# Performance work log

Hardware: AMD Instinct MI355X
Metric: run time of the kernel (lower is better)

The kernel has to match this reference:

```python
import jax, jax.numpy as jnp
import numpy as np

EPS = 1e-5
K = 20

def knn_idx(x, k):
    # x: (B, C, N); returns indices of k nearest neighbors (incl. self), (B, N, k)
    xx = jnp.sum(x * x, axis=1, keepdims=True)            # (B,1,N)
    inner = -2.0 * jnp.einsum('bcn,bcm->bnm', x, x)       # (B,N,N)
    d = -jnp.swapaxes(xx, 1, 2) - inner - xx              # -||xi - xj||^2
    return jax.lax.top_k(d, k)[1]

def graph_feature(x, k):
    # x: (B, C, N) -> (B, 2C, N, k) with [neighbor - center, center]
    B, C, N = x.shape
    idx = knn_idx(x, k)                                   # (B,N,k)
    feat = jnp.swapaxes(x, 1, 2)                          # (B,N,C)
    nb = jax.vmap(lambda f, i: f[i])(feat, idx)           # (B,N,k,C) gather
    ctr = jnp.broadcast_to(feat[:, :, None, :], nb.shape)
    out = jnp.concatenate([nb - ctr, ctr], axis=-1)       # (B,N,k,2C)
    return jnp.transpose(out, (0, 3, 1, 2))

def bn(x, g, b, m, v):
    # inference-mode batchnorm over channel axis 1
    shape = (1, -1) + (1,) * (x.ndim - 2)
    inv = g / jnp.sqrt(v + EPS)
    return x * inv.reshape(shape) + (b - m * inv).reshape(shape)

def edge_block(x, W, g, b, m, v):
    f = graph_feature(x, K)                               # (B,2C,N,k)
    h = jnp.einsum('bcnk,oc->bonk', f, W)                 # 1x1 conv, no bias
    h = jax.nn.relu(bn(h, g, b, m, v))
    return jnp.max(h, axis=-1)                            # max over k -> (B,O,N)

def _forward(x, W1, W2, W3, W4, W5,
             g1, b1, m1, v1, g2, b2, m2, v2, g3, b3, m3, v3,
             g4, b4, m4, v4, g5, b5, m5, v5, g6, b6, m6, v6,
             g7, b7, m7, v7, L1W, L2W, L2b, L3W, L3b):
    x1 = edge_block(x, W1, g1, b1, m1, v1)                # (B,64,N)
    x2 = edge_block(x1, W2, g2, b2, m2, v2)               # (B,64,N)
    x3 = edge_block(x2, W3, g3, b3, m3, v3)               # (B,128,N)
    x4 = edge_block(x3, W4, g4, b4, m4, v4)               # (B,256,N)
    cat = jnp.concatenate([x1, x2, x3, x4], axis=1)       # (B,512,N)
    h = jnp.einsum('bcn,oc->bon', cat, W5)                # conv5 1x1
    h = jax.nn.relu(bn(h, g5, b5, m5, v5))
    h = jnp.max(h, axis=-1)                               # adaptive max pool -> (B,1024)
    h = jax.nn.relu(bn(h @ L1W.T, g6, b6, m6, v6))        # dropout = identity (eval)
    h = jax.nn.relu(bn(h @ L2W.T + L2b, g7, b7, m7, v7))
    return h @ L3W.T + L3b                                # (B, num_classes)

def _bn_params(keys, c):
    k0, k1, k2, k3 = keys
    g = jax.random.uniform(k0, (c,), jnp.float32, 0.5, 1.5)
    b = 0.1 * jax.random.normal(k1, (c,), jnp.float32)
    m = 0.1 * jax.random.normal(k2, (c,), jnp.float32)
    v = jax.random.uniform(k3, (c,), jnp.float32, 0.5, 1.5)
    return g, b, m, v

def setup_inputs() -> dict:
    key = jax.random.key(0)
    ks = jax.random.split(key, 40)
    d = {}
    d['x'] = jax.random.normal(ks[0], (8, 4, 1024), jnp.float32)
    def w(k, o, i):
        return jax.random.normal(k, (o, i), jnp.float32) * np.float32(np.sqrt(2.0 / i))
    d['W1'] = w(ks[1], 64, 8)
    d['W2'] = w(ks[2], 64, 128)
    d['W3'] = w(ks[3], 128, 128)
    d['W4'] = w(ks[4], 256, 256)
    d['W5'] = w(ks[5], 1024, 512)
    for i, c in enumerate([64, 64, 128, 256, 1024, 512, 256]):
        g, b, m, v = _bn_params(jax.random.split(ks[6 + i], 4), c)
        d[f'g{i+1}'], d[f'b{i+1}'], d[f'm{i+1}'], d[f'v{i+1}'] = g, b, m, v
    d['L1W'] = w(ks[20], 512, 1024)
    d['L2W'] = w(ks[21], 256, 512)
    d['L2b'] = 0.1 * jax.random.normal(ks[22], (256,), jnp.float32)
    d['L3W'] = w(ks[23], 8, 256)
    d['L3b'] = 0.1 * jax.random.normal(ks[24], (8,), jnp.float32)
    return d

def reference(x, W1, W2, W3, W4, W5,
              g1, b1, m1, v1, g2, b2, m2, v2, g3, b3, m3, v3,
              g4, b4, m4, v4, g5, b5, m5, v5, g6, b6, m6, v6,
              g7, b7, m7, v7, L1W, L2W, L2b, L3W, L3b):
    return _forward(x, W1, W2, W3, W4, W5,
                    g1, b1, m1, v1, g2, b2, m2, v2, g3, b3, m3, v3,
                    g4, b4, m4, v4, g5, b5, m5, v5, g6, b6, m6, v6,
                    g7, b7, m7, v7, L1W, L2W, L2b, L3W, L3b)
```

## Files before the change

kernel.cpp:

```cpp
#include <hip/hip_runtime.h>
#include <cstdint>

#define BB 8
#define NN 1024
#define KK 20
#define EPSV 1e-5f

typedef __attribute__((ext_vector_type(8))) short bf16x8;
typedef __attribute__((ext_vector_type(4))) float f32x4;

__device__ __forceinline__ unsigned fenc(float f) {
  unsigned u = __float_as_uint(f);
  return (u & 0x80000000u) ? ~u : (u | 0x80000000u);
}
__device__ __forceinline__ float fdec(unsigned u) {
  u = (u & 0x80000000u) ? (u & 0x7FFFFFFFu) : ~u;
  return __uint_as_float(u);
}
__device__ __forceinline__ unsigned short f2bf(float f) {
  unsigned u = __float_as_uint(f);
  unsigned r = u + 0x7FFFu + ((u >> 16) & 1u);
  return (unsigned short)(r >> 16);
}
__device__ __forceinline__ unsigned mbcnt64(unsigned long long m) {
  unsigned r = __builtin_amdgcn_mbcnt_lo((unsigned)m, 0u);
  return __builtin_amdgcn_mbcnt_hi((unsigned)(m >> 32), r);
}

template<int C>
__global__ __launch_bounds__(256) void xx_kernel(const float* __restrict__ x, float* __restrict__ xx) {
  int p = blockIdx.x * 256 + threadIdx.x;
  if (p >= BB * NN) return;
  int b = p >> 10, n = p & (NN - 1);
  const float* xb = x + (size_t)b * C * NN + n;
  float s = 0.f;
  #pragma unroll
  for (int c = 0; c < C; ++c) { float t = xb[(size_t)c * NN]; s = fmaf(t, t, s); }
  xx[p] = s;
}

template<int C>
__global__ __launch_bounds__(256) void dist_kernel(const float* __restrict__ x, const float* __restrict__ xx,
                                                   float* __restrict__ d, int b0) {
  constexpr int CC = (C < 32) ? C : 32;
  __shared__ __align__(16) float xi[CC][64];
  __shared__ __align__(16) float xj[CC][64];
  int bl = blockIdx.z, b = b0 + bl;
  int i0 = blockIdx.y * 64, j0 = blockIdx.x * 64;
  int t = threadIdx.x;
  int tj = t & 15, ti = t >> 4;
  float acc[4][4] = {};
  const float* xb = x + (size_t)b * C * NN;
  for (int c0 = 0; c0 < C; c0 += CC) {
    __syncthreads();
    for (int p = t; p < CC * 16; p += 256) {
      int cc = p >> 4, col = (p & 15) * 4;
      *reinterpret_cast<float4*>(&xi[cc][col]) =
        *reinterpret_cast<const float4*>(&xb[(size_t)(c0 + cc) * NN + i0 + col]);
      *reinterpret_cast<float4*>(&xj[cc][col]) =
        *reinterpret_cast<const float4*>(&xb[(size_t)(c0 + cc) * NN + j0 + col]);
    }
    __syncthreads();
    #pragma unroll
    for (int cc = 0; cc < CC; ++cc) {
      float4 A  = *reinterpret_cast<const float4*>(&xi[cc][ti * 4]);
      float4 Bv = *reinterpret_cast<const float4*>(&xj[cc][tj * 4]);
      float av[4] = {A.x, A.y, A.z, A.w};
      float bv[4] = {Bv.x, Bv.y, Bv.z, Bv.w};
      #pragma unroll
      for (int a = 0; a < 4; ++a)
        #pragma unroll
        for (int q = 0; q < 4; ++q)
          acc[a][q] = fmaf(av[a], bv[q], acc[a][q]);
    }
  }
  #pragma unroll
  for (int a = 0; a < 4; ++a) {
    int i = i0 + ti * 4 + a;
    float xxi = xx[b * NN + i];
    float4 o;
    o.x = 2.f * acc[a][0] - xxi - xx[b * NN + j0 + tj * 4 + 0];
    o.y = 2.f * acc[a][1] - xxi - xx[b * NN + j0 + tj * 4 + 1];
    o.z = 2.f * acc[a][2] - xxi - xx[b * NN + j0 + tj * 4 + 2];
    o.w = 2.f * acc[a][3] - xxi - xx[b * NN + j0 + tj * 4 + 3];
    *reinterpret_cast<float4*>(&d[((size_t)bl * NN + i) * NN + j0 + tj * 4]) = o;
  }
}

__global__ __launch_bounds__(256) void topk_kernel(const float* __restrict__ d, int* __restrict__ idx, int b0) {
  int t = threadIdx.x;
  int wave = t >> 6, lane = t & 63;
  int bl = blockIdx.y, b = b0 + bl;
  int i = blockIdx.x * 4 + wave;
  const float* row = d + ((size_t)bl * NN + i) * NN;

  unsigned v[16];
  #pragma unroll
  for (int p = 0; p < 4; ++p) {
    float4 f = *reinterpret_cast<const float4*>(&row[p * 256 + lane * 4]);
    v[p * 4 + 0] = fenc(f.x);
    v[p * 4 + 1] = fenc(f.y);
    v[p * 4 + 2] = fenc(f.z);
    v[p * 4 + 3] = fenc(f.w);
  }

  unsigned long long lo = 0, hi = 0xFFFFFFFFull;
  while (lo < hi) {
    unsigned long long mid = lo + ((hi - lo + 1) >> 1);
    unsigned mt = (unsigned)mid;
    int c = 0;
    #pragma unroll
    for (int e = 0; e < 16; ++e)
      c += __popcll(__ballot(v[e] >= mt));
    if (c >= KK) lo = mid; else hi = mid - 1;
  }
  unsigned T = (unsigned)lo;

  int* op = idx + ((size_t)b * NN + i) * KK;
  int base = 0, n1 = 0;
  #pragma unroll
  for (int e = 0; e < 16; ++e) {
    unsigned long long mask = __ballot(v[e] > T);
    unsigned mb = mbcnt64(mask);
    if (v[e] > T) op[base + mb] = (e >> 2) * 256 + lane * 4 + (e & 3);
    base += __popcll(mask);
  }
  n1 = base;
  int need = KK - n1;
  int neq = 0;
  #pragma unroll
  for (int e = 0; e < 16; ++e) neq += __popcll(__ballot(v[e] == T));
  if (neq == need) {
    #pragma unroll
    for (int e = 0; e < 16; ++e) {
      unsigned long long mask = __ballot(v[e] == T);
      unsigned mb = mbcnt64(mask);
      if (v[e] == T) op[base + mb] = (e >> 2) * 256 + lane * 4 + (e & 3);
      base += __popcll(mask);
    }
  } else {
    unsigned taken = 0;
    for (int s = 0; s < need; ++s) {
      int jm = 1 << 30;
      #pragma unroll
      for (int e = 0; e < 16; ++e) {
        if (v[e] == T && !((taken >> e) & 1u)) {
          int j = (e >> 2) * 256 + lane * 4 + (e & 3);
          jm = jm < j ? jm : j;
        }
      }
      #pragma unroll
      for (int st = 1; st < 64; st <<= 1) {
        int oj = __shfl_xor(jm, st);
        jm = jm < oj ? jm : oj;
      }
      if (lane == ((jm >> 2) & 63)) {
        int e = (((jm >> 8) << 2) | (jm & 3));
        taken |= 1u << e;
        op[base + s] = jm;
      }
    }
  }
}

template<int C, int O>
__global__ __launch_bounds__(256) void pgemm_kernel(const float* __restrict__ x, const float* __restrict__ W,
                                                    float* __restrict__ Plo, float* __restrict__ Phi) {
  constexpr int CC = (C < 64) ? C : 64;
  __shared__ __align__(16) float xs[CC][64];
  __shared__ __align__(16) float wls[CC][68];
  __shared__ __align__(16) float whs[CC][68];
  int b = blockIdx.z;
  int o0 = blockIdx.y * 64, n0 = blockIdx.x * 64;
  int t = threadIdx.x;
  int tn = t & 15, to = t >> 4;
  float accl[4][4] = {}, acch[4][4] = {};
  const float* xb = x + (size_t)b * C * NN;
  for (int c0 = 0; c0 < C; c0 += CC) {
    __syncthreads();
    for (int p = t; p < CC * 64; p += 256) {
      int cc = p >> 6, col = p & 63;
      xs[cc][col] = xb[(size_t)(c0 + cc) * NN + n0 + col];
    }
    for (int p = t; p < 64 * CC; p += 256) {
      int ol = p / CC, cc = p % CC;
      wls[cc][ol] = W[(size_t)(o0 + ol) * (2 * C) + c0 + cc];
      whs[cc][ol] = W[(size_t)(o0 + ol) * (2 * C) + C + c0 + cc];
    }
    __syncthreads();
    #pragma unroll
    for (int cc = 0; cc < CC; ++cc) {
      float4 X  = *reinterpret_cast<const float4*>(&xs[cc][tn * 4]);
      float4 Wl = *reinterpret_cast<const float4*>(&wls[cc][to * 4]);
      float4 Wh = *reinterpret_cast<const float4*>(&whs[cc][to * 4]);
      float xv[4] = {X.x, X.y, X.z, X.w};
      float wl[4] = {Wl.x, Wl.y, Wl.z, Wl.w};
      float wh[4] = {Wh.x, Wh.y, Wh.z, Wh.w};
      #pragma unroll
      for (int a = 0; a < 4; ++a)
        #pragma unroll
        for (int q = 0; q < 4; ++q) {
          accl[a][q] = fmaf(wl[a], xv[q], accl[a][q]);
          acch[a][q] = fmaf(wh[a], xv[q], acch[a][q]);
        }
    }
  }
  #pragma unroll
  for (int a = 0; a < 4; ++a) {
    int o = o0 + to * 4 + a;
    size_t base = ((size_t)b * O + o) * NN + n0 + tn * 4;
    float4 vl = {accl[a][0], accl[a][1], accl[a][2], accl[a][3]};
    float4 vh = {acch[a][0], acch[a][1], acch[a][2], acch[a][3]};
    *reinterpret_cast<float4*>(&Plo[base]) = vl;
    *reinterpret_cast<float4*>(&Phi[base]) = vh;
  }
}

__global__ __launch_bounds__(256) void edgemax_kernel(const float* __restrict__ Plo, const float* __restrict__ Phi,
    const int* __restrict__ idx, const float* __restrict__ g, const float* __restrict__ bt,
    const float* __restrict__ m, const float* __restrict__ v,
    float* __restrict__ xout, int O) {
  __shared__ __align__(16) float srow[2][NN];
  __shared__ __align__(16) float sphi[2][64];
  __shared__ int   sidx[64 * KK];
  __shared__ float sinv[32], ssb[32];
  int b = blockIdx.z, n0 = blockIdx.y * 64, o0 = blockIdx.x * 32;
  int t = threadIdx.x;
  if (t < 32) {
    float inv = g[o0 + t] / sqrtf(v[o0 + t] + EPSV);
    sinv[t] = inv; ssb[t] = bt[o0 + t] - m[o0 + t] * inv;
  }
  for (int p = t; p < 64 * KK; p += 256) sidx[p] = idx[((size_t)b * NN + n0) * KK + p];
  const float* plobase = Plo + (size_t)b * O * NN;
  const float* phibase = Phi + (size_t)b * O * NN;
  float4 cur0 = *reinterpret_cast<const float4*>(&plobase[(size_t)(o0 + 0) * NN + t * 4]);
  float4 cur1 = *reinterpret_cast<const float4*>(&plobase[(size_t)(o0 + 1) * NN + t * 4]);
  float4 curphi;
  if (t < 32) curphi = *reinterpret_cast<const float4*>(&phibase[(size_t)(o0 + (t >> 4)) * NN + n0 + (t & 15) * 4]);
  __syncthreads();
  int n = t >> 2, kg = t & 3;
  int j0 = sidx[n * KK + kg * 5 + 0];
  int j1 = sidx[n * KK + kg * 5 + 1];
  int j2 = sidx[n * KK + kg * 5 + 2];
  int j3 = sidx[n * KK + kg * 5 + 3];
  int j4 = sidx[n * KK + kg * 5 + 4];
  for (int oo = 0; oo < 32; oo += 2) {
    *reinterpret_cast<float4*>(&srow[0][t * 4]) = cur0;
    *reinterpret_cast<float4*>(&srow[1][t * 4]) = cur1;
    if (t < 32) *reinterpret_cast<float4*>(&sphi[t >> 4][(t & 15) * 4]) = curphi;
    if (oo < 30) {
      cur0 = *reinterpret_cast<const float4*>(&plobase[(size_t)(o0 + oo + 2) * NN + t * 4]);
      cur1 = *reinterpret_cast<const float4*>(&plobase[(size_t)(o0 + oo + 3) * NN + t * 4]);
      if (t < 32) curphi = *reinterpret_cast<const float4*>(&phibase[(size_t)(o0 + oo + 2 + (t >> 4)) * NN + n0 + (t & 15) * 4]);
    }
    __syncthreads();
    float mx0 = srow[0][j0];
    mx0 = fmaxf(mx0, srow[0][j1]);
    mx0 = fmaxf(mx0, srow[0][j2]);
    mx0 = fmaxf(mx0, srow[0][j3]);
    mx0 = fmaxf(mx0, srow[0][j4]);
    float mx1 = srow[1][j0];
    mx1 = fmaxf(mx1, srow[1][j1]);
    mx1 = fmaxf(mx1, srow[1][j2]);
    mx1 = fmaxf(mx1, srow[1][j3]);
    mx1 = fmaxf(mx1, srow[1][j4]);
    mx0 = fmaxf(mx0, __shfl_xor(mx0, 1));
    mx0 = fmaxf(mx0, __shfl_xor(mx0, 2));
    mx1 = fmaxf(mx1, __shfl_xor(mx1, 1));
    mx1 = fmaxf(mx1, __shfl_xor(mx1, 2));
    if (kg == 0) {
      float z0 = mx0 - srow[0][n0 + n] + sphi[0][n];
      float z1 = mx1 - srow[1][n0 + n] + sphi[1][n];
      xout[((size_t)b * O + o0 + oo) * NN + n0 + n]     = fmaxf(fmaf(z0, sinv[oo],     ssb[oo]),     0.f);
      xout[((size_t)b * O + o0 + oo + 1) * NN + n0 + n] = fmaxf(fmaf(z1, sinv[oo + 1], ssb[oo + 1]), 0.f);
    }
    __syncthreads();
  }
}

__global__ __launch_bounds__(256) void tcvt_kernel(const float* __restrict__ src,
    unsigned short* __restrict__ dst, int Csrc, int c0) {
  __shared__ float tile[64][65];
  int b = blockIdx.z, cb = blockIdx.y * 64, n0 = blockIdx.x * 64;
  int t = threadIdx.x;
  const float* s = src + ((size_t)b * Csrc + cb) * NN + n0;
  #pragma unroll
  for (int rr = 0; rr < 4; ++rr) {
    int r = (t >> 4) + rr * 16;
    float4 v = *reinterpret_cast<const float4*>(&s[(size_t)r * NN + (t & 15) * 4]);
    tile[r][(t & 15) * 4 + 0] = v.x;
    tile[r][(t & 15) * 4 + 1] = v.y;
    tile[r][(t & 15) * 4 + 2] = v.z;
    tile[r][(t & 15) * 4 + 3] = v.w;
  }
  __syncthreads();
  #pragma unroll
  for (int rr = 0; rr < 2; ++rr) {
    int chunk = t + 256 * rr;
    int n = chunk >> 3, cg = (chunk & 7) * 8;
    unsigned short u[8];
    #pragma unroll
    for (int j = 0; j < 8; ++j) u[j] = f2bf(tile[cg + j][n]);
    *reinterpret_cast<uint4*>(&dst[((size_t)b * NN + n0 + n) * 512 + c0 + cb + cg]) =
      *reinterpret_cast<const uint4*>(u);
  }
}

__global__ __launch_bounds__(256) void cvtw_kernel(const float* __restrict__ W, unsigned short* __restrict__ Wb) {
  int p = (blockIdx.x * 256 + threadIdx.x) * 4;
  float4 v = *reinterpret_cast<const float4*>(&W[p]);
  unsigned short u[4] = {f2bf(v.x), f2bf(v.y), f2bf(v.z), f2bf(v.w)};
  *reinterpret_cast<uint2*>(&Wb[p]) = *reinterpret_cast<const uint2*>(u);
}

__global__ __launch_bounds__(256) void pgemm4_mfma_kernel(const unsigned short* __restrict__ Xb,
    const unsigned short* __restrict__ W4b, float* __restrict__ Plo_t, float* __restrict__ Phi_t) {
  int b = blockIdx.z;
  int n0 = blockIdx.x * 128, o0 = blockIdx.y * 64;
  int t = threadIdx.x, lane = t & 63, w = t >> 6;
  int r = lane & 15, kc = lane >> 4;
  const unsigned short* A  = Xb + ((size_t)b * NN + n0 + w * 32 + r) * 512 + 128 + kc * 8;
  const unsigned short* Bw = W4b + ((size_t)(o0 + r)) * 256 + kc * 8;
  f32x4 accl0[4] = {}, accl1[4] = {}, acch0[4] = {}, acch1[4] = {};
  #pragma unroll
  for (int ks = 0; ks < 128; ks += 32) {
    bf16x8 a0 = *reinterpret_cast<const bf16x8*>(A + ks);
    bf16x8 a1 = *reinterpret_cast<const bf16x8*>(A + 16 * 512 + ks);
    #pragma unroll
    for (int j = 0; j < 4; ++j) {
      bf16x8 bl = *reinterpret_cast<const bf16x8*>(Bw + (size_t)j * 16 * 256 + ks);
      bf16x8 bh = *reinterpret_cast<const bf16x8*>(Bw + (size_t)j * 16 * 256 + 128 + ks);
      accl0[j] = __builtin_amdgcn_mfma_f32_16x16x32_bf16(a0, bl, accl0[j], 0, 0, 0);
      accl1[j] = __builtin_amdgcn_mfma_f32_16x16x32_bf16(a1, bl, accl1[j], 0, 0, 0);
      acch0[j] = __builtin_amdgcn_mfma_f32_16x16x32_bf16(a0, bh, acch0[j], 0, 0, 0);
      acch1[j] = __builtin_amdgcn_mfma_f32_16x16x32_bf16(a1, bh, acch1[j], 0, 0, 0);
    }
  }
  #pragma unroll
  for (int j = 0; j < 4; ++j) {
    #pragma unroll
    for (int reg = 0; reg < 4; ++reg) {
      size_t n_a = (size_t)b * NN + n0 + w * 32 + kc * 4 + reg;
      size_t n_b = n_a + 16;
      int oc = o0 + j * 16 + r;
      Plo_t[n_a * 256 + oc] = accl0[j][reg];
      Plo_t[n_b * 256 + oc] = accl1[j][reg];
      Phi_t[n_a * 256 + oc] = acch0[j][reg];
      Phi_t[n_b * 256 + oc] = acch1[j][reg];
    }
  }
}

__global__ __launch_bounds__(256) void edgemax4_kernel(const float* __restrict__ Plo_t,
    const float* __restrict__ Phi_t, const int* __restrict__ idx,
    const float* __restrict__ g, const float* __restrict__ bt,
    const float* __restrict__ m, const float* __restrict__ v,
    unsigned short* __restrict__ Xb) {
  int b = blockIdx.y, t = threadIdx.x;
  int n = blockIdx.x * 4 + (t >> 6);
  int oc = (t & 63) * 4;
  const int* ip = idx + ((size_t)b * NN + n) * KK;
  const float* base = Plo_t + (size_t)b * NN * 256;
  float4 mx = {-3.4e38f, -3.4e38f, -3.4e38f, -3.4e38f};
  #pragma unroll
  for (int k = 0; k < KK; ++k) {
    float4 vv = *reinterpret_cast<const float4*>(base + (size_t)ip[k] * 256 + oc);
    mx.x = fmaxf(mx.x, vv.x);
    mx.y = fmaxf(mx.y, vv.y);
    mx.z = fmaxf(mx.z, vv.z);
    mx.w = fmaxf(mx.w, vv.w);
  }
  float4 self = *reinterpret_cast<const float4*>(base + (size_t)n * 256 + oc);
  float4 ph = *reinterpret_cast<const float4*>(Phi_t + ((size_t)b * NN + n) * 256 + oc);
  float4 gg = *reinterpret_cast<const float4*>(g + oc);
  float4 bb = *reinterpret_cast<const float4*>(bt + oc);
  float4 mm = *reinterpret_cast<const float4*>(m + oc);
  float4 vv4 = *reinterpret_cast<const float4*>(v + oc);
  float mxa[4] = {mx.x, mx.y, mx.z, mx.w};
  float sfa[4] = {self.x, self.y, self.z, self.w};
  float pha[4] = {ph.x, ph.y, ph.z, ph.w};
  float ga[4] = {gg.x, gg.y, gg.z, gg.w};
  float ba[4] = {bb.x, bb.y, bb.z, bb.w};
  float ma[4] = {mm.x, mm.y, mm.z, mm.w};
  float va[4] = {vv4.x, vv4.y, vv4.z, vv4.w};
  unsigned short u[4];
  #pragma unroll
  for (int e = 0; e < 4; ++e) {
    float inv = ga[e] / sqrtf(va[e] + EPSV);
    float z = mxa[e] - sfa[e] + pha[e];
    float y = fmaxf(fmaf(z, inv, ba[e] - ma[e] * inv), 0.f);
    u[e] = f2bf(y);
  }
  *reinterpret_cast<uint2*>(&Xb[((size_t)b * NN + n) * 512 + 256 + oc]) =
    *reinterpret_cast<const uint2*>(u);
}

__global__ __launch_bounds__(256) void conv5_mfma_kernel(const unsigned short* __restrict__ Xb,
    const unsigned short* __restrict__ W5b, unsigned* __restrict__ henc) {
  int b = blockIdx.z;
  int n0 = blockIdx.x * 128, o0 = blockIdx.y * 64;
  int t = threadIdx.x, lane = t & 63, w = t >> 6;
  int r = lane & 15, kc = lane >> 4;
  const unsigned short* A = W5b + ((size_t)(o0 + r)) * 512 + kc * 8;
  const unsigned short* B = Xb + ((size_t)b * NN + n0 + w * 32 + r) * 512 + kc * 8;
  f32x4 acc00 = {}, acc01 = {}, acc10 = {}, acc11 = {};
  f32x4 acc20 = {}, acc21 = {}, acc30 = {}, acc31 = {};
  bf16x8 a0 = *reinterpret_cast<const bf16x8*>(A + 0 * 16 * 512);
  bf16x8 a1 = *reinterpret_cast<const bf16x8*>(A + 1 * 16 * 512);
  bf16x8 a2 = *reinterpret_cast<const bf16x8*>(A + 2 * 16 * 512);
  bf16x8 a3 = *reinterpret_cast<const bf16x8*>(A + 3 * 16 * 512);
  bf16x8 b0 = *reinterpret_cast<const bf16x8*>(B);
  bf16x8 b1 = *reinterpret_cast<const bf16x8*>(B + 16 * 512);
  #pragma unroll
  for (int ks = 0; ks < 512; ks += 32) {
    bf16x8 na0, na1, na2, na3, nb0, nb1;
    if (ks + 32 < 512) {
      na0 = *reinterpret_cast<const bf16x8*>(A + 0 * 16 * 512 + ks + 32);
      na1 = *reinterpret_cast<const bf16x8*>(A + 1 * 16 * 512 + ks + 32);
      na2 = *reinterpret_cast<const bf16x8*>(A + 2 * 16 * 512 + ks + 32);
      na3 = *reinterpret_cast<const bf16x8*>(A + 3 * 16 * 512 + ks + 32);
      nb0 = *reinterpret_cast<const bf16x8*>(B + ks + 32);
      nb1 = *reinterpret_cast<const bf16x8*>(B + 16 * 512 + ks + 32);
    }
    acc00 = __builtin_amdgcn_mfma_f32_16x16x32_bf16(a0, b0, acc00, 0, 0, 0);
    acc01 = __builtin_amdgcn_mfma_f32_16x16x32_bf16(a0, b1, acc01, 0, 0, 0);
    acc10 = __builtin_amdgcn_mfma_f32_16x16x32_bf16(a1, b0, acc10, 0, 0, 0);
    acc11 = __builtin_amdgcn_mfma_f32_16x16x32_bf16(a1, b1, acc11, 0, 0, 0);
    acc20 = __builtin_amdgcn_mfma_f32_16x16x32_bf16(a2, b0, acc20, 0, 0, 0);
    acc21 = __builtin_amdgcn_mfma_f32_16x16x32_bf16(a2, b1, acc21, 0, 0, 0);
    acc30 = __builtin_amdgcn_mfma_f32_16x16x32_bf16(a3, b0, acc30, 0, 0, 0);
    acc31 = __builtin_amdgcn_mfma_f32_16x16x32_bf16(a3, b1, acc31, 0, 0, 0);
    a0 = na0; a1 = na1; a2 = na2; a3 = na3; b0 = nb0; b1 = nb1;
  }
  f32x4 m0 = {fmaxf(acc00[0], acc01[0]), fmaxf(acc00[1], acc01[1]),
              fmaxf(acc00[2], acc01[2]), fmaxf(acc00[3], acc01[3])};
  f32x4 m1 = {fmaxf(acc10[0], acc11[0]), fmaxf(acc10[1], acc11[1]),
              fmaxf(acc10[2], acc11[2]), fmaxf(acc10[3], acc11[3])};
  f32x4 m2 = {fmaxf(acc20[0], acc21[0]), fmaxf(acc20[1], acc21[1]),
              fmaxf(acc20[2], acc21[2]), fmaxf(acc20[3], acc21[3])};
  f32x4 m3 = {fmaxf(acc30[0], acc31[0]), fmaxf(acc30[1], acc31[1]),
              fmaxf(acc30[2], acc31[2]), fmaxf(acc30[3], acc31[3])};
  #pragma unroll
  for (int st = 1; st < 16; st <<= 1) {
    #pragma unroll
    for (int reg = 0; reg < 4; ++reg) {
      m0[reg] = fmaxf(m0[reg], __shfl_xor(m0[reg], st));
      m1[reg] = fmaxf(m1[reg], __shfl_xor(m1[reg], st));
      m2[reg] = fmaxf(m2[reg], __shfl_xor(m2[reg], st));
      m3[reg] = fmaxf(m3[reg], __shfl_xor(m3[reg], st));
    }
  }
  if (r == 0) {
    #pragma unroll
    for (int reg = 0; reg < 4; ++reg) {
      atomicMax(&henc[b * 1024 + o0 + 0 * 16 + kc * 4 + reg], fenc(m0[reg]));
      atomicMax(&henc[b * 1024 + o0 + 1 * 16 + kc * 4 + reg], fenc(m1[reg]));
      atomicMax(&henc[b * 1024 + o0 + 2 * 16 + kc * 4 + reg], fenc(m2[reg]));
      atomicMax(&henc[b * 1024 + o0 + 3 * 16 + kc * 4 + reg], fenc(m3[reg]));
    }
  }
}

__global__ __launch_bounds__(256) void fc1_kernel(
    const unsigned* __restrict__ henc,
    const float* __restrict__ g5, const float* __restrict__ b5, const float* __restrict__ m5, const float* __restrict__ v5,
    const float* __restrict__ L1W,
    const float* __restrict__ g6, const float* __restrict__ b6, const float* __restrict__ m6, const float* __restrict__ v6,
    float* __restrict__ y1) {
  __shared__ float sh[1024];
  int b = blockIdx.y, t = threadIdx.x;
  int o0 = blockIdx.x * 64;
  for (int o = t; o < 1024; o += 256) {
    float f = fdec(henc[b * 1024 + o]);
    float inv = g5[o] / sqrtf(v5[o] + EPSV);
    sh[o] = fmaxf(fmaf(f, inv, b5[o] - m5[o] * inv), 0.f);
  }
  __syncthreads();
  int o = o0 + (t >> 2), part = t & 3;
  float acc = 0.f;
  const float4* w4 = reinterpret_cast<const float4*>(L1W + (size_t)o * 1024 + part * 256);
  const float4* h4 = reinterpret_cast<const float4*>(sh + part * 256);
  #pragma unroll 8
  for (int c = 0; c < 64; ++c) {
    float4 a = w4[c], q = h4[c];
    acc = fmaf(a.x, q.x, fmaf(a.y, q.y, fmaf(a.z, q.z, fmaf(a.w, q.w, acc))));
  }
  acc += __shfl_xor(acc, 1);
  acc += __shfl_xor(acc, 2);
  if (part == 0) {
    float inv = g6[o] / sqrtf(v6[o] + EPSV);
    y1[b * 512 + o] = fmaxf(fmaf(acc, inv, b6[o] - m6[o] * inv), 0.f);
  }
}

__global__ __launch_bounds__(256) void fc2_kernel(
    const float* __restrict__ y1,
    const float* __restrict__ L2W, const float* __restrict__ L2b,
    const float* __restrict__ g7, const float* __restrict__ b7, const float* __restrict__ m7, const float* __restrict__ v7,
    const float* __restrict__ L3W, const float* __restrict__ L3b,
    float* __restrict__ out) {
  __shared__ float sy1[512];
  __shared__ float sy2[256];
  int b = blockIdx.x, t = threadIdx.x;
  for (int o = t; o < 512; o += 256) sy1[o] = y1[b * 512 + o];
  __syncthreads();
  {
    int o = t;
    float acc = L2b[o];
    const float4* w4 = reinterpret_cast<const float4*>(L2W + (size_t)o * 512);
    const float4* q4 = reinterpret_cast<const float4*>(sy1);
    for (int c = 0; c < 128; ++c) {
      float4 a = w4[c], q = q4[c];
      acc = fmaf(a.x, q.x, fmaf(a.y, q.y, fmaf(a.z, q.z, fmaf(a.w, q.w, acc))));
    }
    float inv = g7[o] / sqrtf(v7[o] + EPSV);
    sy2[o] = fmaxf(fmaf(acc, inv, b7[o] - m7[o] * inv), 0.f);
  }
  __syncthreads();
  if (t < 8) {
    float acc = L3b[t];
    const float4* w4 = reinterpret_cast<const float4*>(L3W + (size_t)t * 256);
    const float4* q4 = reinterpret_cast<const float4*>(sy2);
    for (int c = 0; c < 64; ++c) {
      float4 a = w4[c], q = q4[c];
      acc = fmaf(a.x, q.x, fmaf(a.y, q.y, fmaf(a.z, q.z, fmaf(a.w, q.w, acc))));
    }
    out[b * 8 + t] = acc;
  }
}

extern "C" void kernel_launch(void* const* d_in, const int* in_sizes, int n_in,
                              void* d_out, int out_size, void* d_ws, size_t ws_size,
                              hipStream_t stream) {
  (void)in_sizes; (void)n_in; (void)out_size;
  const float* x   = (const float*)d_in[0];
  const float* W1  = (const float*)d_in[1];
  const float* W2  = (const float*)d_in[2];
  const float* W3  = (const float*)d_in[3];
  const float* W4  = (const float*)d_in[4];
  const float* W5  = (const float*)d_in[5];
  const float* bnp[7][4];
  for (int i = 0; i < 7; ++i)
    for (int j = 0; j < 4; ++j)
      bnp[i][j] = (const float*)d_in[6 + i * 4 + j];
  const float* L1W = (const float*)d_in[34];
  const float* L2W = (const float*)d_in[35];
  const float* L2b = (const float*)d_in[36];
  const float* L3W = (const float*)d_in[37];
  const float* L3b = (const float*)d_in[38];
  float* out = (float*)d_out;

  char* wsb = (char*)d_ws;
  size_t off = 0;
  auto alloc = [&](size_t bytes) -> void* {
    void* p = wsb + off; off += (bytes + 255) & ~(size_t)255; return p;
  };
  int*      idx  = (int*)     alloc((size_t)BB * NN * KK * 4);
  float*    xx   = (float*)   alloc((size_t)BB * NN * 4);
  float*    x1   = (float*)   alloc((size_t)BB * 64  * NN * 4);
  float*    x2   = (float*)   alloc((size_t)BB * 64  * NN * 4);
  float*    x3   = (float*)   alloc((size_t)BB * 128 * NN * 4);
  float*    Plo  = (float*)   alloc((size_t)BB * 256 * NN * 4);
  float*    Phi  = (float*)   alloc((size_t)BB * 256 * NN * 4);
  unsigned* henc = (unsigned*)alloc((size_t)BB * 1024 * 4);
  float*    y1   = (float*)   alloc((size_t)BB * 512 * 4);
  unsigned short* Xb  = (unsigned short*)alloc((size_t)BB * NN * 512 * 2);
  unsigned short* W5b = (unsigned short*)alloc((size_t)1024 * 512 * 2);
  unsigned short* W4b = (unsigned short*)alloc((size_t)256 * 256 * 2);
  size_t left = (ws_size > off) ? (ws_size - off) : 0;
  int nb = 8;
  while (nb > 1 && (size_t)nb * NN * NN * 4 > left) nb >>= 1;
  float* dbuf = (float*)(wsb + off);

  dim3 thr(256);
  #define KNN_PHASE(CIN, XIN)                                                              \
    xx_kernel<CIN><<<dim3(32), thr, 0, stream>>>(XIN, xx);                                 \
    for (int b0 = 0; b0 < BB; b0 += nb) {                                                  \
      dist_kernel<CIN><<<dim3(16, 16, nb), thr, 0, stream>>>(XIN, xx, dbuf, b0);           \
      topk_kernel<<<dim3(NN / 4, nb), thr, 0, stream>>>(dbuf, idx, b0);                    \
    }

  cvtw_kernel<<<dim3(512), thr, 0, stream>>>(W5, W5b);
  cvtw_kernel<<<dim3(64), thr, 0, stream>>>(W4, W4b);

  KNN_PHASE(4, x)
  pgemm_kernel<4, 64><<<dim3(16, 1, BB), thr, 0, stream>>>(x, W1, Plo, Phi);
  edgemax_kernel<<<dim3(2, 16, BB), thr, 0, stream>>>(Plo, Phi, idx,
      bnp[0][0], bnp[0][1], bnp[0][2], bnp[0][3], x1, 64);
  tcvt_kernel<<<dim3(16, 1, BB), thr, 0, stream>>>(x1, Xb, 64, 0);
  KNN_PHASE(64, x1)
  pgemm_kernel<64, 64><<<dim3(16, 1, BB), thr, 0, stream>>>(x1, W2, Plo, Phi);
  edgemax_kernel<<<dim3(2, 16, BB), thr, 0, stream>>>(Plo, Phi, idx,
      bnp[1][0], bnp[1][1], bnp[1][2], bnp[1][3], x2, 64);
  tcvt_kernel<<<dim3(16, 1, BB), thr, 0, stream>>>(x2, Xb, 64, 64);
  KNN_PHASE(64, x2)
  pgemm_kernel<64, 128><<<dim3(16, 2, BB), thr, 0, stream>>>(x2, W3, Plo, Phi);
  edgemax_kernel<<<dim3(4, 16, BB), thr, 0, stream>>>(Plo, Phi, idx,
      bnp[2][0], bnp[2][1], bnp[2][2], bnp[2][3], x3, 128);
  tcvt_kernel<<<dim3(16, 2, BB), thr, 0, stream>>>(x3, Xb, 128, 128);
  KNN_PHASE(128, x3)
  pgemm4_mfma_kernel<<<dim3(8, 4, BB), thr, 0, stream>>>(Xb, W4b, Plo, Phi);
  edgemax4_kernel<<<dim3(256, BB), thr, 0, stream>>>(Plo, Phi, idx,
      bnp[3][0], bnp[3][1], bnp[3][2], bnp[3][3], Xb);
  #undef KNN_PHASE

  hipMemsetAsync(henc, 0, (size_t)BB * 1024 * 4, stream);
  conv5_mfma_kernel<<<dim3(8, 16, BB), thr, 0, stream>>>(Xb, W5b, henc);

  fc1_kernel<<<dim3(8, BB), thr, 0, stream>>>(henc,
      bnp[4][0], bnp[4][1], bnp[4][2], bnp[4][3], L1W,
      bnp[5][0], bnp[5][1], bnp[5][2], bnp[5][3], y1);
  fc2_kernel<<<dim3(BB), thr, 0, stream>>>(y1,
      L2W, L2b, bnp[6][0], bnp[6][1], bnp[6][2], bnp[6][3], L3W, L3b, out);
}
```

Baseline: 437.7 us.

## Stage conv5 weight tile in LDS and preload all activation fragments

The conv5 MFMA kernel now loads the block's 64x512 bf16 weight tile into shared memory once, stored in the MFMA fragment order, so the four waves share it instead of each fetching it from global memory. Each wave also preloads all sixteen K-step activation fragments into registers up front, replacing the one-step software prefetch. This is meant to cut redundant global weight traffic and load latency stalls. In exchange it uses 64KB of LDS and many more VGPRs, with launch bounds set to one block per SM, which lowers occupancy.

```diff
diff --git a/kernel.cpp b/kernel.cpp
--- a/kernel.cpp
+++ b/kernel.cpp
@@ -395,43 +395,49 @@
     *reinterpret_cast<const uint2*>(u);
 }
 
-__global__ __launch_bounds__(256) void conv5_mfma_kernel(const unsigned short* __restrict__ Xb,
+__global__ __launch_bounds__(256, 1) void conv5_mfma_kernel(const unsigned short* __restrict__ Xb,
     const unsigned short* __restrict__ W5b, unsigned* __restrict__ henc) {
+  __shared__ __align__(16) unsigned short lA[4096 * 8];
   int b = blockIdx.z;
   int n0 = blockIdx.x * 128, o0 = blockIdx.y * 64;
   int t = threadIdx.x, lane = t & 63, w = t >> 6;
   int r = lane & 15, kc = lane >> 4;
-  const unsigned short* A = W5b + ((size_t)(o0 + r)) * 512 + kc * 8;
+
   const unsigned short* B = Xb + ((size_t)b * NN + n0 + w * 32 + r) * 512 + kc * 8;
+  bf16x8 b0[16], b1[16];
+  #pragma unroll
+  for (int ks = 0; ks < 16; ++ks) {
+    b0[ks] = *reinterpret_cast<const bf16x8*>(B + ks * 32);
+    b1[ks] = *reinterpret_cast<const bf16x8*>(B + 16 * 512 + ks * 32);
+  }
+
+  #pragma unroll
+  for (int i = 0; i < 16; ++i) {
+    int e = i * 256 + t;
+    int le = e & 63, je = (e >> 6) & 3, kse = e >> 8;
+    const unsigned short* src = W5b + ((size_t)(o0 + je * 16 + (le & 15))) * 512 + ((le >> 4) & 3) * 8 + kse * 32;
+    *reinterpret_cast<uint4*>(&lA[(size_t)e * 8]) = *reinterpret_cast<const uint4*>(src);
+  }
+  __syncthreads();
+
   f32x4 acc00 = {}, acc01 = {}, acc10 = {}, acc11 = {};
   f32x4 acc20 = {}, acc21 = {}, acc30 = {}, acc31 = {};
-  bf16x8 a0 = *reinterpret_cast<const bf16x8*>(A + 0 * 16 * 512);
-  bf16x8 a1 = *reinterpret_cast<const bf16x8*>(A + 1 * 16 * 512);
-  bf16x8 a2 = *reinterpret_cast<const bf16x8*>(A + 2 * 16 * 512);
-  bf16x8 a3 = *reinterpret_cast<const bf16x8*>(A + 3 * 16 * 512);
-  bf16x8 b0 = *reinterpret_cast<const bf16x8*>(B);
-  bf16x8 b1 = *reinterpret_cast<const bf16x8*>(B + 16 * 512);
-  #pragma unroll
-  for (int ks = 0; ks < 512; ks += 32) {
-    bf16x8 na0, na1, na2, na3, nb0, nb1;
-    if (ks + 32 < 512) {
-      na0 = *reinterpret_cast<const bf16x8*>(A + 0 * 16 * 512 + ks + 32);
-      na1 = *reinterpret_cast<const bf16x8*>(A + 1 * 16 * 512 + ks + 32);
-      na2 = *reinterpret_cast<const bf16x8*>(A + 2 * 16 * 512 + ks + 32);
-      na3 = *reinterpret_cast<const bf16x8*>(A + 3 * 16 * 512 + ks + 32);
-      nb0 = *reinterpret_cast<const bf16x8*>(B + ks + 32);
-      nb1 = *reinterpret_cast<const bf16x8*>(B + 16 * 512 + ks + 32);
-    }
-    acc00 = __builtin_amdgcn_mfma_f32_16x16x32_bf16(a0, b0, acc00, 0, 0, 0);
-    acc01 = __builtin_amdgcn_mfma_f32_16x16x32_bf16(a0, b1, acc01, 0, 0, 0);
-    acc10 = __builtin_amdgcn_mfma_f32_16x16x32_bf16(a1, b0, acc10, 0, 0, 0);
-    acc11 = __builtin_amdgcn_mfma_f32_16x16x32_bf16(a1, b1, acc11, 0, 0, 0);
-    acc20 = __builtin_amdgcn_mfma_f32_16x16x32_bf16(a2, b0, acc20, 0, 0, 0);
-    acc21 = __builtin_amdgcn_mfma_f32_16x16x32_bf16(a2, b1, acc21, 0, 0, 0);
-    acc30 = __builtin_amdgcn_mfma_f32_16x16x32_bf16(a3, b0, acc30, 0, 0, 0);
-    acc31 = __builtin_amdgcn_mfma_f32_16x16x32_bf16(a3, b1, acc31, 0, 0, 0);
-    a0 = na0; a1 = na1; a2 = na2; a3 = na3; b0 = nb0; b1 = nb1;
-  }
+  #pragma unroll
+  for (int ks = 0; ks < 16; ++ks) {
+    bf16x8 a0 = *reinterpret_cast<const bf16x8*>(&lA[(size_t)((ks * 4 + 0) * 64 + lane) * 8]);
+    bf16x8 a1 = *reinterpret_cast<const bf16x8*>(&lA[(size_t)((ks * 4 + 1) * 64 + lane) * 8]);
+    bf16x8 a2 = *reinterpret_cast<const bf16x8*>(&lA[(size_t)((ks * 4 + 2) * 64 + lane) * 8]);
+    bf16x8 a3 = *reinterpret_cast<const bf16x8*>(&lA[(size_t)((ks * 4 + 3) * 64 + lane) * 8]);
+    acc00 = __builtin_amdgcn_mfma_f32_16x16x32_bf16(a0, b0[ks], acc00, 0, 0, 0);
+    acc01 = __builtin_amdgcn_mfma_f32_16x16x32_bf16(a0, b1[ks], acc01, 0, 0, 0);
+    acc10 = __builtin_amdgcn_mfma_f32_16x16x32_bf16(a1, b0[ks], acc10, 0, 0, 0);
+    acc11 = __builtin_amdgcn_mfma_f32_16x16x32_bf16(a1, b1[ks], acc11, 0, 0, 0);
+    acc20 = __builtin_amdgcn_mfma_f32_16x16x32_bf16(a2, b0[ks], acc20, 0, 0, 0);
+    acc21 = __builtin_amdgcn_mfma_f32_16x16x32_bf16(a2, b1[ks], acc21, 0, 0, 0);
+    acc30 = __builtin_amdgcn_mfma_f32_16x16x32_bf16(a3, b0[ks], acc30, 0, 0, 0);
+    acc31 = __builtin_amdgcn_mfma_f32_16x16x32_bf16(a3, b1[ks], acc31, 0, 0, 0);
+  }
+
   f32x4 m0 = {fmaxf(acc00[0], acc01[0]), fmaxf(acc00[1], acc01[1]),
               fmaxf(acc00[2], acc01[2]), fmaxf(acc00[3], acc01[3])};
   f32x4 m1 = {fmaxf(acc10[0], acc11[0]), fmaxf(acc10[1], acc11[1]),
```

Measured after the change: 419.5 us, median of 2. 4.1% less time.
